# Kernel optimization log

Measured on AMD Instinct MI355X. Metric: run time of the kernel, lower is better.

Reference implementation:

```python
import jax, jax.numpy as jnp
import numpy as np

SEARCH_RANGE = 4  # max_displacement; kernel_size=1, strides=1, pad=search_range
LEAKY_SLOPE = 0.1


def setup_inputs() -> dict:
    key = jax.random.key(0)
    k1, k2 = jax.random.split(key)
    B, H, W, C = 8, 128, 128, 192
    prv = jax.random.normal(k1, (B, H, W, C), dtype=jnp.float32)
    nxt = jax.random.normal(k2, (B, H, W, C), dtype=jnp.float32)
    return {"prv": prv, "nxt": nxt}


def _cost_volume(prv, nxt, d):
    # tfa CorrelationCost with kernel_size=1: for each displacement (dy, dx) in
    # [-d, d]^2, out[b,y,x,k] = mean_c prv[b,y,x,c] * nxt[b,y+dy,x+dx,c],
    # with zero padding of nxt by d. Displacements ordered row-major (dy outer).
    B, H, W, C = prv.shape
    nxt_p = jnp.pad(nxt, ((0, 0), (d, d), (d, d), (0, 0)))
    outs = []
    for dy in range(2 * d + 1):  # fixed small set (9)
        for dx in range(2 * d + 1):
            shifted = nxt_p[:, dy:dy + H, dx:dx + W, :]  # [B,H,W,C]
            outs.append(jnp.mean(prv * shifted, axis=-1))  # [B,H,W]
    return jnp.stack(outs, axis=-1)  # [B,H,W,81]


def reference(prv, nxt):
    cv = _cost_volume(prv, nxt, SEARCH_RANGE)
    return jax.nn.leaky_relu(cv, LEAKY_SLOPE)
```

## Files before the change

kernel.cpp:

```cpp
#include <hip/hip_runtime.h>
#include <hip/hip_bf16.h>


#define B_ 8
#define H_ 128
#define W_ 128
#define C_ 192
#define ND 9
#define NDISP 81
#define HT 16
#define WT 16
#define KS 32
#define NK 6
#define BROWS 24
#define BCOLS 24
#define APIX (HT * WT)
#define BPIX (BROWS * BCOLS)
#define ASTR 257
#define BSTR 577
#define ASLOTS (8 * ASTR)
#define BSLOTS (8 * BSTR)
#define NSA 2
#define NSB 5

typedef short short8 __attribute__((ext_vector_type(8)));
typedef short short4_t __attribute__((ext_vector_type(4)));
typedef float f32x4 __attribute__((ext_vector_type(4)));

static __device__ __forceinline__ short bf1(float f) {
    __hip_bfloat16 h = __float2bfloat16(f);
    return __builtin_bit_cast(short, h);
}

static __device__ __forceinline__ short4_t cvt4(float4 v) {
    short4_t r;
    r[0] = bf1(v.x); r[1] = bf1(v.y); r[2] = bf1(v.z); r[3] = bf1(v.w);
    return r;
}

static __device__ __forceinline__ short8 cat(short4_t u, short4_t v) {
    return __builtin_shufflevector(u, v, 0, 1, 2, 3, 4, 5, 6, 7);
}

static __device__ __forceinline__ void barrier_no_vm_drain() {
    asm volatile("s_waitcnt lgkmcnt(0)\n\ts_barrier" ::: "memory");
}

__global__ __launch_bounds__(1024, 4)
void cv_mfma(const float* __restrict__ prv, const float* __restrict__ nxt,
             float* __restrict__ out) {
    __shared__ short4_t sm[2][ASLOTS + BSLOTS];

    const int tid = threadIdx.x;
    const int w0 = blockIdx.x * WT;
    const int h0 = blockIdx.y * HT;
    const int b  = blockIdx.z;

    const int lane = tid & 63;
    const int wid  = tid >> 6;
    const int lq = lane & 15;
    const int lc = lane >> 4;

    const int tp = tid >> 3;
    const int c8 = tid & 7;

    int aoff[NSA];
#pragma unroll
    for (int i = 0; i < NSA; ++i) {
        const int p = tp + 128 * i;
        const int r = p >> 4;
        const int pc = p & 15;
        aoff[i] = ((b * H_ + h0 + r) * W_ + w0 + pc) * C_ + c8 * 4;
    }
    int boff[NSB];
    unsigned bmask = 0;
#pragma unroll
    for (int i = 0; i < NSB; ++i) {
        const int p = tp + 128 * i;
        const int row = p / BCOLS;
        const int col = p - row * BCOLS;
        const int gh = h0 - 4 + row;
        const int gw = w0 - 4 + col;
        const bool inb = (p < BPIX) && ((unsigned)gh < (unsigned)H_) && ((unsigned)gw < (unsigned)W_);
        if (inb) bmask |= (1u << i);
        boff[i] = ((b * H_ + (inb ? gh : 0)) * W_ + (inb ? gw : 0)) * C_ + c8 * 4;
    }
    const bool wr4 = (tid < 512);

    float4 xa[NSA], xb[NSB];

#pragma unroll
    for (int i = 0; i < NSA; ++i) xa[i] = *(const float4*)(prv + aoff[i]);
#pragma unroll
    for (int i = 0; i < NSB; ++i) {
        xb[i] = make_float4(0.f, 0.f, 0.f, 0.f);
        if (bmask & (1u << i)) xb[i] = *(const float4*)(nxt + boff[i]);
    }

    f32x4 acc[ND][2];
#pragma unroll
    for (int d = 0; d < ND; ++d) {
        acc[d][0] = (f32x4){0.f, 0.f, 0.f, 0.f};
        acc[d][1] = (f32x4){0.f, 0.f, 0.f, 0.f};
    }

    for (int it = 0; it < NK; ++it) {
        short4_t* sA = sm[it & 1];
        short4_t* sB = sm[it & 1] + ASLOTS;

#pragma unroll
        for (int i = 0; i < NSA; ++i)
            sA[c8 * ASTR + tp + 128 * i] = cvt4(xa[i]);
#pragma unroll
        for (int i = 0; i < NSB - 1; ++i)
            sB[c8 * BSTR + tp + 128 * i] = cvt4(xb[i]);
        if (wr4)
            sB[c8 * BSTR + tp + 128 * (NSB - 1)] = cvt4(xb[NSB - 1]);

        if (it + 1 < NK) {
            const int co = (it + 1) * KS;
#pragma unroll
            for (int i = 0; i < NSA; ++i) xa[i] = *(const float4*)(prv + aoff[i] + co);
#pragma unroll
            for (int i = 0; i < NSB; ++i) {
                if (bmask & (1u << i)) xb[i] = *(const float4*)(nxt + boff[i] + co);
            }
        }

        barrier_no_vm_drain();

        const int pA = wid * WT + lq;
        const short8 a = cat(sA[2 * lc * ASTR + pA], sA[(2 * lc + 1) * ASTR + pA]);
#pragma unroll
        for (int dy = 0; dy < ND; ++dy) {
            const int pB = (wid + dy) * BCOLS + lq;
            const short8 b0 = cat(sB[2 * lc * BSTR + pB],     sB[(2 * lc + 1) * BSTR + pB]);
            const short8 b1 = cat(sB[2 * lc * BSTR + pB + 8], sB[(2 * lc + 1) * BSTR + pB + 8]);
            acc[dy][0] = __builtin_amdgcn_mfma_f32_16x16x32_bf16(a, b0, acc[dy][0], 0, 0, 0);
            acc[dy][1] = __builtin_amdgcn_mfma_f32_16x16x32_bf16(a, b1, acc[dy][1], 0, 0, 0);
        }
    }

    const float inv = 1.0f / (float)C_;
    const int h = h0 + wid;
    if (lc < 2) {
#pragma unroll
        for (int rg = 0; rg < 4; ++rg) {
            const int r = 4 * lc + rg;
            const int dx = lq - r;
            if (dx >= 0 && dx <= 8) {
                float* o = out + (size_t)((b * H_ + h) * W_ + w0 + r) * NDISP + dx;
#pragma unroll
                for (int dy = 0; dy < ND; ++dy) {
                    const float v = acc[dy][0][rg] * inv;
                    o[dy * ND] = v >= 0.f ? v : 0.1f * v;
                }
            }
        }
    } else {
#pragma unroll
        for (int rg = 0; rg < 4; ++rg) {
            const int r = 4 * lc + rg;
            const int dx = lq - r + 8;
            if (dx >= 0 && dx <= 8) {
                float* o = out + (size_t)((b * H_ + h) * W_ + w0 + r) * NDISP + dx;
#pragma unroll
                for (int dy = 0; dy < ND; ++dy) {
                    const float v = acc[dy][1][rg] * inv;
                    o[dy * ND] = v >= 0.f ? v : 0.1f * v;
                }
            }
        }
    }
}

extern "C" void kernel_launch(void* const* d_in, const int* in_sizes, int n_in,
                              void* d_out, int out_size, void* d_ws, size_t ws_size,
                              hipStream_t stream) {
    const float* prv = (const float*)d_in[0];
    const float* nxt = (const float*)d_in[1];
    float* out = (float*)d_out;

    dim3 grid(W_ / WT, H_ / HT, B_);
    cv_mfma<<<grid, 1024, 0, stream>>>(prv, nxt, out);
}
```

Baseline: 77.50 us.

## Load A fragments directly to registers, prefetch B two stages ahead, stagger channel order

The A tile no longer goes through shared memory. Each lane loads its own 8 channels of prv straight into registers and converts them to the bf16 MFMA fragment. The B tile loads are now double-buffered in registers two chunks ahead, and the chunk loop is fully unrolled. The starting channel chunk is rotated per block, spreading simultaneous DRAM/L2 accesses across channel offsets. The aim is lower LDS traffic and footprint and more latency hiding, at the cost of more registers (two B register sets) and less coalesced 32-byte A loads.

Result: slower. 144.4 us (+86.3%).

```diff
diff --git a/kernel.cpp b/kernel.cpp
--- a/kernel.cpp
+++ b/kernel.cpp
@@ -14,13 +14,9 @@
 #define NK 6
 #define BROWS 24
 #define BCOLS 24
-#define APIX (HT * WT)
 #define BPIX (BROWS * BCOLS)
-#define ASTR 257
 #define BSTR 577
-#define ASLOTS (8 * ASTR)
 #define BSLOTS (8 * BSTR)
-#define NSA 2
 #define NSB 5
 
 typedef short short8 __attribute__((ext_vector_type(8)));
@@ -42,6 +38,12 @@
     return __builtin_shufflevector(u, v, 0, 1, 2, 3, 4, 5, 6, 7);
 }
 
+static __device__ __forceinline__ int mod6(int v) {
+    v -= (v >= 6) ? 6 : 0;
+    v -= (v >= 6) ? 6 : 0;
+    return v;
+}
+
 static __device__ __forceinline__ void barrier_no_vm_drain() {
     asm volatile("s_waitcnt lgkmcnt(0)\n\ts_barrier" ::: "memory");
 }
@@ -49,7 +51,7 @@
 __global__ __launch_bounds__(1024, 4)
 void cv_mfma(const float* __restrict__ prv, const float* __restrict__ nxt,
              float* __restrict__ out) {
-    __shared__ short4_t sm[2][ASLOTS + BSLOTS];
+    __shared__ short4_t sm[2][BSLOTS];
 
     const int tid = threadIdx.x;
     const int w0 = blockIdx.x * WT;
@@ -64,14 +66,6 @@
     const int tp = tid >> 3;
     const int c8 = tid & 7;
 
-    int aoff[NSA];
-#pragma unroll
-    for (int i = 0; i < NSA; ++i) {
-        const int p = tp + 128 * i;
-        const int r = p >> 4;
-        const int pc = p & 15;
-        aoff[i] = ((b * H_ + h0 + r) * W_ + w0 + pc) * C_ + c8 * 4;
-    }
     int boff[NSB];
     unsigned bmask = 0;
 #pragma unroll
@@ -87,14 +81,27 @@
     }
     const bool wr4 = (tid < 512);
 
-    float4 xa[NSA], xb[NSB];
+    const int aoff = ((b * H_ + h0 + wid) * W_ + w0 + lq) * C_ + lc * 8;
 
+    const int start = mod6((int)(blockIdx.x + blockIdx.y + blockIdx.z) % 12);
+
+    float4 xa0, xa1;
+    float4 xb0[NSB], xb1[NSB];
+    {
+        const int c0 = start * KS;
+        xa0 = *(const float4*)(prv + aoff + c0);
+        xa1 = *(const float4*)(prv + aoff + c0 + 4);
 #pragma unroll
-    for (int i = 0; i < NSA; ++i) xa[i] = *(const float4*)(prv + aoff[i]);
+        for (int i = 0; i < NSB; ++i) {
+            xb0[i] = make_float4(0.f, 0.f, 0.f, 0.f);
+            if (bmask & (1u << i)) xb0[i] = *(const float4*)(nxt + boff[i] + c0);
+        }
+        const int c1 = mod6(start + 1) * KS;
 #pragma unroll
-    for (int i = 0; i < NSB; ++i) {
-        xb[i] = make_float4(0.f, 0.f, 0.f, 0.f);
-        if (bmask & (1u << i)) xb[i] = *(const float4*)(nxt + boff[i]);
+        for (int i = 0; i < NSB; ++i) {
+            xb1[i] = make_float4(0.f, 0.f, 0.f, 0.f);
+            if (bmask & (1u << i)) xb1[i] = *(const float4*)(nxt + boff[i] + c1);
+        }
     }
 
     f32x4 acc[ND][2];
@@ -104,42 +111,46 @@
         acc[d][1] = (f32x4){0.f, 0.f, 0.f, 0.f};
     }
 
-    for (int it = 0; it < NK; ++it) {
-        short4_t* sA = sm[it & 1];
-        short4_t* sB = sm[it & 1] + ASLOTS;
+#define PHASE(IT, XB)                                                              \
+    {                                                                              \
+        short4_t* sB = sm[IT & 1];                                                 \
+                        \
+        _Pragma("unroll")                                                          \
+        for (int i = 0; i < NSB - 1; ++i)                                          \
+            sB[c8 * BSTR + tp + 128 * i] = cvt4(XB[i]);                            \
+        if (wr4) sB[c8 * BSTR + tp + 512] = cvt4(XB[NSB - 1]);                     \
+                         \
+        const short8 afrag = cat(cvt4(xa0), cvt4(xa1));                            \
+        if (IT + 1 < NK) {                                      \
+            const int cn = mod6(start + IT + 1) * KS;                              \
+            xa0 = *(const float4*)(prv + aoff + cn);                               \
+            xa1 = *(const float4*)(prv + aoff + cn + 4);                           \
+        }                                                                          \
+        if (IT + 2 < NK) {            \
+            const int cb = mod6(start + IT + 2) * KS;                              \
+            _Pragma("unroll")                                                      \
+            for (int i = 0; i < NSB; ++i) {                                        \
+                if (bmask & (1u << i)) XB[i] = *(const float4*)(nxt + boff[i] + cb); \
+            }                                                                      \
+        }                                                                          \
+        barrier_no_vm_drain();                                                     \
+        _Pragma("unroll")                                                          \
+        for (int dy = 0; dy < ND; ++dy) {                                          \
+            const int pB = (wid + dy) * BCOLS + lq;                                \
+            const short8 b0v = cat(sB[2 * lc * BSTR + pB], sB[(2 * lc + 1) * BSTR + pB]); \
+            const short8 b1v = cat(sB[2 * lc * BSTR + pB + 8], sB[(2 * lc + 1) * BSTR + pB + 8]); \
+            acc[dy][0] = __builtin_amdgcn_mfma_f32_16x16x32_bf16(afrag, b0v, acc[dy][0], 0, 0, 0); \
+            acc[dy][1] = __builtin_amdgcn_mfma_f32_16x16x32_bf16(afrag, b1v, acc[dy][1], 0, 0, 0); \
+        }                                                                          \
+    }
 
-#pragma unroll
-        for (int i = 0; i < NSA; ++i)
-            sA[c8 * ASTR + tp + 128 * i] = cvt4(xa[i]);
-#pragma unroll
-        for (int i = 0; i < NSB - 1; ++i)
-            sB[c8 * BSTR + tp + 128 * i] = cvt4(xb[i]);
-        if (wr4)
-            sB[c8 * BSTR + tp + 128 * (NSB - 1)] = cvt4(xb[NSB - 1]);
-
-        if (it + 1 < NK) {
-            const int co = (it + 1) * KS;
-#pragma unroll
-            for (int i = 0; i < NSA; ++i) xa[i] = *(const float4*)(prv + aoff[i] + co);
-#pragma unroll
-            for (int i = 0; i < NSB; ++i) {
-                if (bmask & (1u << i)) xb[i] = *(const float4*)(nxt + boff[i] + co);
-            }
-        }
-
-        barrier_no_vm_drain();
-
-        const int pA = wid * WT + lq;
-        const short8 a = cat(sA[2 * lc * ASTR + pA], sA[(2 * lc + 1) * ASTR + pA]);
-#pragma unroll
-        for (int dy = 0; dy < ND; ++dy) {
-            const int pB = (wid + dy) * BCOLS + lq;
-            const short8 b0 = cat(sB[2 * lc * BSTR + pB],     sB[(2 * lc + 1) * BSTR + pB]);
-            const short8 b1 = cat(sB[2 * lc * BSTR + pB + 8], sB[(2 * lc + 1) * BSTR + pB + 8]);
-            acc[dy][0] = __builtin_amdgcn_mfma_f32_16x16x32_bf16(a, b0, acc[dy][0], 0, 0, 0);
-            acc[dy][1] = __builtin_amdgcn_mfma_f32_16x16x32_bf16(a, b1, acc[dy][1], 0, 0, 0);
-        }
-    }
+    PHASE(0, xb0)
+    PHASE(1, xb1)
+    PHASE(2, xb0)
+    PHASE(3, xb1)
+    PHASE(4, xb0)
+    PHASE(5, xb1)
+#undef PHASE
 
     const float inv = 1.0f / (float)C_;
     const int h = h0 + wid;
```

## Load A fragments directly to registers and split B prefetch across MFMA phases

Applied to the files above, without the earlier changes.

Drops the shared-memory staging of the prv tile: each lane now loads its A fragment directly from global memory into registers and converts it to bf16. The channel chunk per iteration doubles to 64, giving 3 iterations instead of 6 and so fewer barriers. The next chunk's nxt loads are split into two groups issued between the two halves of the MFMA loop, so global latency overlaps with compute. This raises register pressure and LDS use per block, which could lower occupancy under the 1024-thread launch bound.

Result: faster. 75.22 us (-2.9%).

```diff
diff --git a/kernel.cpp b/kernel.cpp
--- a/kernel.cpp
+++ b/kernel.cpp
@@ -10,18 +10,16 @@
 #define NDISP 81
 #define HT 16
 #define WT 16
-#define KS 32
-#define NK 6
+#define KS 64
+#define NK 3
 #define BROWS 24
 #define BCOLS 24
-#define APIX (HT * WT)
 #define BPIX (BROWS * BCOLS)
-#define ASTR 257
 #define BSTR 577
-#define ASLOTS (8 * ASTR)
-#define BSLOTS (8 * BSTR)
-#define NSA 2
-#define NSB 5
+#define BSLOTS (16 * BSTR)
+#define NSB 9
+#define NB1 5
+#define NB2 4
 
 typedef short short8 __attribute__((ext_vector_type(8)));
 typedef short short4_t __attribute__((ext_vector_type(4)));
@@ -42,14 +40,14 @@
     return __builtin_shufflevector(u, v, 0, 1, 2, 3, 4, 5, 6, 7);
 }
 
-static __device__ __forceinline__ void barrier_no_vm_drain() {
+static __device__ __forceinline__ void barrier_lgkm() {
     asm volatile("s_waitcnt lgkmcnt(0)\n\ts_barrier" ::: "memory");
 }
 
 __global__ __launch_bounds__(1024, 4)
 void cv_mfma(const float* __restrict__ prv, const float* __restrict__ nxt,
              float* __restrict__ out) {
-    __shared__ short4_t sm[2][ASLOTS + BSLOTS];
+    __shared__ short4_t sm[2][BSLOTS];
 
     const int tid = threadIdx.x;
     const int w0 = blockIdx.x * WT;
@@ -61,40 +59,40 @@
     const int lq = lane & 15;
     const int lc = lane >> 4;
 
-    const int tp = tid >> 3;
-    const int c8 = tid & 7;
-
-    int aoff[NSA];
-#pragma unroll
-    for (int i = 0; i < NSA; ++i) {
-        const int p = tp + 128 * i;
-        const int r = p >> 4;
-        const int pc = p & 15;
-        aoff[i] = ((b * H_ + h0 + r) * W_ + w0 + pc) * C_ + c8 * 4;
-    }
+    const int tp  = tid >> 4;
+    const int c16 = tid & 15;
+
     int boff[NSB];
     unsigned bmask = 0;
 #pragma unroll
     for (int i = 0; i < NSB; ++i) {
-        const int p = tp + 128 * i;
+        const int p = tp + 64 * i;
         const int row = p / BCOLS;
         const int col = p - row * BCOLS;
         const int gh = h0 - 4 + row;
         const int gw = w0 - 4 + col;
-        const bool inb = (p < BPIX) && ((unsigned)gh < (unsigned)H_) && ((unsigned)gw < (unsigned)W_);
+        const bool inb = ((unsigned)gh < (unsigned)H_) && ((unsigned)gw < (unsigned)W_);
         if (inb) bmask |= (1u << i);
-        boff[i] = ((b * H_ + (inb ? gh : 0)) * W_ + (inb ? gw : 0)) * C_ + c8 * 4;
-    }
-    const bool wr4 = (tid < 512);
-
-    float4 xa[NSA], xb[NSB];
-
-#pragma unroll
-    for (int i = 0; i < NSA; ++i) xa[i] = *(const float4*)(prv + aoff[i]);
-#pragma unroll
-    for (int i = 0; i < NSB; ++i) {
-        xb[i] = make_float4(0.f, 0.f, 0.f, 0.f);
-        if (bmask & (1u << i)) xb[i] = *(const float4*)(nxt + boff[i]);
+        boff[i] = ((b * H_ + (inb ? gh : 0)) * W_ + (inb ? gw : 0)) * C_ + c16 * 4;
+    }
+
+    const int aoff = ((b * H_ + h0 + wid) * W_ + w0 + lq) * C_ + lc * 8;
+
+    float4 xa[4];
+    xa[0] = *(const float4*)(prv + aoff);
+    xa[1] = *(const float4*)(prv + aoff + 4);
+    xa[2] = *(const float4*)(prv + aoff + 32);
+    xa[3] = *(const float4*)(prv + aoff + 36);
+    {
+        float4 v[NSB];
+#pragma unroll
+        for (int i = 0; i < NSB; ++i) {
+            v[i] = make_float4(0.f, 0.f, 0.f, 0.f);
+            if (bmask & (1u << i)) v[i] = *(const float4*)(nxt + boff[i]);
+        }
+#pragma unroll
+        for (int i = 0; i < NSB; ++i)
+            sm[0][c16 * BSTR + tp + 64 * i] = cvt4(v[i]);
     }
 
     f32x4 acc[ND][2];
@@ -104,41 +102,73 @@
         acc[d][1] = (f32x4){0.f, 0.f, 0.f, 0.f};
     }
 
+    barrier_lgkm();
+
     for (int it = 0; it < NK; ++it) {
-        short4_t* sA = sm[it & 1];
-        short4_t* sB = sm[it & 1] + ASLOTS;
-
-#pragma unroll
-        for (int i = 0; i < NSA; ++i)
-            sA[c8 * ASTR + tp + 128 * i] = cvt4(xa[i]);
-#pragma unroll
-        for (int i = 0; i < NSB - 1; ++i)
-            sB[c8 * BSTR + tp + 128 * i] = cvt4(xb[i]);
-        if (wr4)
-            sB[c8 * BSTR + tp + 128 * (NSB - 1)] = cvt4(xb[NSB - 1]);
-
-        if (it + 1 < NK) {
-            const int co = (it + 1) * KS;
-#pragma unroll
-            for (int i = 0; i < NSA; ++i) xa[i] = *(const float4*)(prv + aoff[i] + co);
-#pragma unroll
-            for (int i = 0; i < NSB; ++i) {
-                if (bmask & (1u << i)) xb[i] = *(const float4*)(nxt + boff[i] + co);
-            }
-        }
-
-        barrier_no_vm_drain();
-
-        const int pA = wid * WT + lq;
-        const short8 a = cat(sA[2 * lc * ASTR + pA], sA[(2 * lc + 1) * ASTR + pA]);
-#pragma unroll
-        for (int dy = 0; dy < ND; ++dy) {
+        short4_t* sBc = sm[it & 1];
+        short4_t* sBn = sm[(it + 1) & 1];
+        const short8 af0 = cat(cvt4(xa[0]), cvt4(xa[1]));
+        const short8 af1 = cat(cvt4(xa[2]), cvt4(xa[3]));
+
+        const bool more = (it + 1 < NK);
+        const int co = (it + 1) * KS;
+
+        float4 v1[NB1];
+#pragma unroll
+        for (int i = 0; i < NB1; ++i) {
+            v1[i] = make_float4(0.f, 0.f, 0.f, 0.f);
+            if (more && (bmask & (1u << i))) v1[i] = *(const float4*)(nxt + boff[i] + co);
+        }
+
+#pragma unroll
+        for (int dy = 0; dy < 5; ++dy) {
             const int pB = (wid + dy) * BCOLS + lq;
-            const short8 b0 = cat(sB[2 * lc * BSTR + pB],     sB[(2 * lc + 1) * BSTR + pB]);
-            const short8 b1 = cat(sB[2 * lc * BSTR + pB + 8], sB[(2 * lc + 1) * BSTR + pB + 8]);
-            acc[dy][0] = __builtin_amdgcn_mfma_f32_16x16x32_bf16(a, b0, acc[dy][0], 0, 0, 0);
-            acc[dy][1] = __builtin_amdgcn_mfma_f32_16x16x32_bf16(a, b1, acc[dy][1], 0, 0, 0);
-        }
+            const short8 b00 = cat(sBc[(2 * lc) * BSTR + pB],     sBc[(2 * lc + 1) * BSTR + pB]);
+            const short8 b01 = cat(sBc[(2 * lc) * BSTR + pB + 8], sBc[(2 * lc + 1) * BSTR + pB + 8]);
+            acc[dy][0] = __builtin_amdgcn_mfma_f32_16x16x32_bf16(af0, b00, acc[dy][0], 0, 0, 0);
+            acc[dy][1] = __builtin_amdgcn_mfma_f32_16x16x32_bf16(af0, b01, acc[dy][1], 0, 0, 0);
+            const short8 b10 = cat(sBc[(8 + 2 * lc) * BSTR + pB],     sBc[(9 + 2 * lc) * BSTR + pB]);
+            const short8 b11 = cat(sBc[(8 + 2 * lc) * BSTR + pB + 8], sBc[(9 + 2 * lc) * BSTR + pB + 8]);
+            acc[dy][0] = __builtin_amdgcn_mfma_f32_16x16x32_bf16(af1, b10, acc[dy][0], 0, 0, 0);
+            acc[dy][1] = __builtin_amdgcn_mfma_f32_16x16x32_bf16(af1, b11, acc[dy][1], 0, 0, 0);
+        }
+
+        if (more) {
+#pragma unroll
+            for (int i = 0; i < NB1; ++i)
+                sBn[c16 * BSTR + tp + 64 * i] = cvt4(v1[i]);
+        }
+        float4 v2[NB2];
+#pragma unroll
+        for (int i = 0; i < NB2; ++i) {
+            v2[i] = make_float4(0.f, 0.f, 0.f, 0.f);
+            if (more && (bmask & (1u << (NB1 + i)))) v2[i] = *(const float4*)(nxt + boff[NB1 + i] + co);
+        }
+
+#pragma unroll
+        for (int dy = 5; dy < ND; ++dy) {
+            const int pB = (wid + dy) * BCOLS + lq;
+            const short8 b00 = cat(sBc[(2 * lc) * BSTR + pB],     sBc[(2 * lc + 1) * BSTR + pB]);
+            const short8 b01 = cat(sBc[(2 * lc) * BSTR + pB + 8], sBc[(2 * lc + 1) * BSTR + pB + 8]);
+            acc[dy][0] = __builtin_amdgcn_mfma_f32_16x16x32_bf16(af0, b00, acc[dy][0], 0, 0, 0);
+            acc[dy][1] = __builtin_amdgcn_mfma_f32_16x16x32_bf16(af0, b01, acc[dy][1], 0, 0, 0);
+            const short8 b10 = cat(sBc[(8 + 2 * lc) * BSTR + pB],     sBc[(9 + 2 * lc) * BSTR + pB]);
+            const short8 b11 = cat(sBc[(8 + 2 * lc) * BSTR + pB + 8], sBc[(9 + 2 * lc) * BSTR + pB + 8]);
+            acc[dy][0] = __builtin_amdgcn_mfma_f32_16x16x32_bf16(af1, b10, acc[dy][0], 0, 0, 0);
+            acc[dy][1] = __builtin_amdgcn_mfma_f32_16x16x32_bf16(af1, b11, acc[dy][1], 0, 0, 0);
+        }
+
+        if (more) {
+#pragma unroll
+            for (int i = 0; i < NB2; ++i)
+                sBn[c16 * BSTR + tp + 64 * (NB1 + i)] = cvt4(v2[i]);
+            xa[0] = *(const float4*)(prv + aoff + co);
+            xa[1] = *(const float4*)(prv + aoff + co + 4);
+            xa[2] = *(const float4*)(prv + aoff + co + 32);
+            xa[3] = *(const float4*)(prv + aoff + co + 36);
+        }
+
+        barrier_lgkm();
     }
 
     const float inv = 1.0f / (float)C_;
```

## Stage nxt tiles via direct global-to-LDS loads, load prv straight to registers

Applied to the files above, without the earlier changes.

Replaces the register round-trip for the nxt halo tile with global_load_lds 16-byte direct copies into shared memory. These keep fp32 in LDS and convert to bf16 after each LDS read. Out-of-bounds pixels read from a zeroed workspace buffer, set by an added memset. The prv operand now goes directly from global into registers in MFMA layout, so the A tile no longer passes through shared memory. This cuts VGPR staging and LDS write instructions, at the cost of doubling LDS traffic (fp32 instead of bf16), repeating conversion work per displacement, and adding a memset launch.

After: 126.8 us. 1.64x slower.

```diff
diff --git a/kernel.cpp b/kernel.cpp
--- a/kernel.cpp
+++ b/kernel.cpp
@@ -12,16 +12,9 @@
 #define WT 16
 #define KS 32
 #define NK 6
-#define BROWS 24
 #define BCOLS 24
-#define APIX (HT * WT)
-#define BPIX (BROWS * BCOLS)
-#define ASTR 257
-#define BSTR 577
-#define ASLOTS (8 * ASTR)
-#define BSLOTS (8 * BSTR)
-#define NSA 2
-#define NSB 5
+#define GRB 9232
+#define BUFB (8 * GRB)
 
 typedef short short8 __attribute__((ext_vector_type(8)));
 typedef short short4_t __attribute__((ext_vector_type(4)));
@@ -42,14 +35,23 @@
     return __builtin_shufflevector(u, v, 0, 1, 2, 3, 4, 5, 6, 7);
 }
 
-static __device__ __forceinline__ void barrier_no_vm_drain() {
-    asm volatile("s_waitcnt lgkmcnt(0)\n\ts_barrier" ::: "memory");
+static __device__ __forceinline__ void gload16(const float* g, char* l) {
+    __builtin_amdgcn_global_load_lds(
+        (const __attribute__((address_space(1))) void*)g,
+        (__attribute__((address_space(3))) void*)l,
+        16, 0, 0);
+}
+
+static __device__ __forceinline__ int lbyte(int g, int px) {
+    return g * GRB + ((px >> 6) << 10) + ((px & 63) << 4);
 }
 
 __global__ __launch_bounds__(1024, 4)
 void cv_mfma(const float* __restrict__ prv, const float* __restrict__ nxt,
+             const float* __restrict__ zp,
              float* __restrict__ out) {
-    __shared__ short4_t sm[2][ASLOTS + BSLOTS];
+    __shared__ char sm[2][BUFB] __attribute__((aligned(16)));
+    char* smb = &sm[0][0];
 
     const int tid = threadIdx.x;
     const int w0 = blockIdx.x * WT;
@@ -61,41 +63,40 @@
     const int lq = lane & 15;
     const int lc = lane >> 4;
 
-    const int tp = tid >> 3;
-    const int c8 = tid & 7;
+    const int nld = (wid < 8) ? 5 : 4;
+    const float* bptr[5];
+    int ldst[5];
+#pragma unroll
+    for (int j = 0; j < 5; ++j) {
+        bptr[j] = zp; ldst[j] = 0;
+        const int i = wid + 16 * j;
+        if (i < 72) {
+            const int g = i / 9;
+            const int c = i - 9 * g;
+            const int px = c * 64 + lane;
+            const int row = px / BCOLS;
+            const int col = px - row * BCOLS;
+            const int gh = h0 - 4 + row;
+            const int gw = w0 - 4 + col;
+            const bool inb = ((unsigned)gh < (unsigned)H_) && ((unsigned)gw < (unsigned)W_);
+            bptr[j] = inb ? (nxt + ((b * H_ + gh) * W_ + gw) * C_ + g * 4) : zp;
+            ldst[j] = g * GRB + c * 1024;
+        }
+    }
 
-    int aoff[NSA];
-#pragma unroll
-    for (int i = 0; i < NSA; ++i) {
-        const int p = tp + 128 * i;
-        const int r = p >> 4;
-        const int pc = p & 15;
-        aoff[i] = ((b * H_ + h0 + r) * W_ + w0 + pc) * C_ + c8 * 4;
+    const int aoff = ((b * H_ + h0 + wid) * W_ + w0 + lq) * C_ + lc * 8;
+
+#define STAGE(KK, BUFN)                                                     \
+    {                                                                       \
+        _Pragma("unroll")                                                   \
+        for (int j = 0; j < 5; ++j)                                         \
+            if (j < nld) gload16(bptr[j] + (KK) * KS, (BUFN) + ldst[j]);    \
     }
-    int boff[NSB];
-    unsigned bmask = 0;
-#pragma unroll
-    for (int i = 0; i < NSB; ++i) {
-        const int p = tp + 128 * i;
-        const int row = p / BCOLS;
-        const int col = p - row * BCOLS;
-        const int gh = h0 - 4 + row;
-        const int gw = w0 - 4 + col;
-        const bool inb = (p < BPIX) && ((unsigned)gh < (unsigned)H_) && ((unsigned)gw < (unsigned)W_);
-        if (inb) bmask |= (1u << i);
-        boff[i] = ((b * H_ + (inb ? gh : 0)) * W_ + (inb ? gw : 0)) * C_ + c8 * 4;
-    }
-    const bool wr4 = (tid < 512);
 
-    float4 xa[NSA], xb[NSB];
-
-#pragma unroll
-    for (int i = 0; i < NSA; ++i) xa[i] = *(const float4*)(prv + aoff[i]);
-#pragma unroll
-    for (int i = 0; i < NSB; ++i) {
-        xb[i] = make_float4(0.f, 0.f, 0.f, 0.f);
-        if (bmask & (1u << i)) xb[i] = *(const float4*)(nxt + boff[i]);
-    }
+    STAGE(0, smb)
+    float4 xa0 = *(const float4*)(prv + aoff);
+    float4 xa1 = *(const float4*)(prv + aoff + 4);
+    asm volatile("s_waitcnt vmcnt(0)\n\ts_barrier" ::: "memory");
 
     f32x4 acc[ND][2];
 #pragma unroll
@@ -105,41 +106,33 @@
     }
 
     for (int it = 0; it < NK; ++it) {
-        short4_t* sA = sm[it & 1];
-        short4_t* sB = sm[it & 1] + ASLOTS;
+        char* bufc = smb + (it & 1) * BUFB;
+        char* bufn = smb + ((it + 1) & 1) * BUFB;
+        const short8 af = cat(cvt4(xa0), cvt4(xa1));
+
+        if (it + 1 < NK) {
+            STAGE(it + 1, bufn)
+            const int co = (it + 1) * KS;
+            xa0 = *(const float4*)(prv + aoff + co);
+            xa1 = *(const float4*)(prv + aoff + co + 4);
+        }
 
 #pragma unroll
-        for (int i = 0; i < NSA; ++i)
-            sA[c8 * ASTR + tp + 128 * i] = cvt4(xa[i]);
-#pragma unroll
-        for (int i = 0; i < NSB - 1; ++i)
-            sB[c8 * BSTR + tp + 128 * i] = cvt4(xb[i]);
-        if (wr4)
-            sB[c8 * BSTR + tp + 128 * (NSB - 1)] = cvt4(xb[NSB - 1]);
-
-        if (it + 1 < NK) {
-            const int co = (it + 1) * KS;
-#pragma unroll
-            for (int i = 0; i < NSA; ++i) xa[i] = *(const float4*)(prv + aoff[i] + co);
-#pragma unroll
-            for (int i = 0; i < NSB; ++i) {
-                if (bmask & (1u << i)) xb[i] = *(const float4*)(nxt + boff[i] + co);
-            }
+        for (int dy = 0; dy < ND; ++dy) {
+            const int p0 = (wid + dy) * BCOLS + lq;
+            const float4 f00 = *(const float4*)(bufc + lbyte(2 * lc, p0));
+            const float4 f01 = *(const float4*)(bufc + lbyte(2 * lc + 1, p0));
+            const float4 f10 = *(const float4*)(bufc + lbyte(2 * lc, p0 + 8));
+            const float4 f11 = *(const float4*)(bufc + lbyte(2 * lc + 1, p0 + 8));
+            const short8 b0 = cat(cvt4(f00), cvt4(f01));
+            const short8 b1 = cat(cvt4(f10), cvt4(f11));
+            acc[dy][0] = __builtin_amdgcn_mfma_f32_16x16x32_bf16(af, b0, acc[dy][0], 0, 0, 0);
+            acc[dy][1] = __builtin_amdgcn_mfma_f32_16x16x32_bf16(af, b1, acc[dy][1], 0, 0, 0);
         }
 
-        barrier_no_vm_drain();
-
-        const int pA = wid * WT + lq;
-        const short8 a = cat(sA[2 * lc * ASTR + pA], sA[(2 * lc + 1) * ASTR + pA]);
-#pragma unroll
-        for (int dy = 0; dy < ND; ++dy) {
-            const int pB = (wid + dy) * BCOLS + lq;
-            const short8 b0 = cat(sB[2 * lc * BSTR + pB],     sB[(2 * lc + 1) * BSTR + pB]);
-            const short8 b1 = cat(sB[2 * lc * BSTR + pB + 8], sB[(2 * lc + 1) * BSTR + pB + 8]);
-            acc[dy][0] = __builtin_amdgcn_mfma_f32_16x16x32_bf16(a, b0, acc[dy][0], 0, 0, 0);
-            acc[dy][1] = __builtin_amdgcn_mfma_f32_16x16x32_bf16(a, b1, acc[dy][1], 0, 0, 0);
-        }
+        asm volatile("s_waitcnt vmcnt(0)\n\ts_barrier" ::: "memory");
     }
+#undef STAGE
 
     const float inv = 1.0f / (float)C_;
     const int h = h0 + wid;
@@ -181,6 +174,8 @@
     const float* nxt = (const float*)d_in[1];
     float* out = (float*)d_out;
 
+    hipMemsetAsync(d_ws, 0, 1024, stream);
+
     dim3 grid(W_ / WT, H_ / HT, B_);
-    cv_mfma<<<grid, 1024, 0, stream>>>(prv, nxt, out);
+    cv_mfma<<<grid, 1024, 0, stream>>>(prv, nxt, (const float*)d_ws, out);
 }
```
